# Kernel tuning notes

Measured on AMD Instinct MI355X. Metric: run time of the kernel, lower is better.

The kernel has to match this reference:

```python
import jax, jax.numpy as jnp
import numpy as np

D_MODEL = 1024
N_HEADS = 16
N_KV = 4
HEAD_DIM = D_MODEL // N_HEADS  # 64
SEQ = 2048
BATCH = 2
CAP = 50.0
EPS = 1e-5
THETA = 10000.0


def setup_inputs() -> dict:
    key = jax.random.key(0)
    ks = jax.random.split(key, 5)
    s = 0.02  # keep pre-attention logits in a sane range
    return {
        'x':   jax.random.normal(ks[0], (BATCH, SEQ, D_MODEL), dtype=jnp.float32),
        'w_q': jax.random.normal(ks[1], (D_MODEL, N_HEADS * HEAD_DIM), dtype=jnp.float32) * s,
        'w_k': jax.random.normal(ks[2], (D_MODEL, N_KV * HEAD_DIM), dtype=jnp.float32) * s,
        'w_v': jax.random.normal(ks[3], (D_MODEL, N_KV * HEAD_DIM), dtype=jnp.float32) * s,
        'w_o': jax.random.normal(ks[4], (N_HEADS * HEAD_DIM, D_MODEL), dtype=jnp.float32) * s,
    }


def _rms_norm(x, eps=EPS):
    return x * jax.lax.rsqrt(jnp.mean(jnp.square(x), axis=-1, keepdims=True) + eps)


def _rope_cos_sin(seq_len, head_dim, theta=THETA):
    inv_freq = 1.0 / (theta ** (jnp.arange(0, head_dim, 2, dtype=jnp.float32) / head_dim))
    freqs = jnp.arange(seq_len, dtype=jnp.float32)[:, None] * inv_freq[None, :]  # (S, d/2)
    return jnp.cos(freqs)[None, :, None, :], jnp.sin(freqs)[None, :, None, :]  # (1,S,1,d/2)


def _apply_rope(x, cos, sin):
    d = x.shape[-1] // 2
    x1, x2 = x[..., :d], x[..., d:]
    return jnp.concatenate([x1 * cos - x2 * sin, x2 * cos + x1 * sin], axis=-1).astype(x.dtype)


def reference(x, w_q, w_k, w_v, w_o):
    B, S, _ = x.shape
    q = (x @ w_q).reshape(B, S, N_HEADS, HEAD_DIM)
    k = (x @ w_k).reshape(B, S, N_KV, HEAD_DIM)
    v = (x @ w_v).reshape(B, S, N_KV, HEAD_DIM)

    # QK RMS-norm (no learned scale)
    q = _rms_norm(q)
    k = _rms_norm(k)

    cos, sin = _rope_cos_sin(S, HEAD_DIM)
    q = _apply_rope(q, cos, sin)
    k = _apply_rope(k, cos, sin)

    # GQA: repeat kv heads to match query heads
    rep = N_HEADS // N_KV
    k = jnp.repeat(k, rep, axis=2)
    v = jnp.repeat(v, rep, axis=2)

    scores = jnp.einsum('bqhd,bkhd->bhqk', q, k) / np.sqrt(HEAD_DIM).astype(np.float32)
    # softcap in float32, as in the original
    scores = jnp.tanh(scores.astype(jnp.float32) / CAP) * CAP
    causal = jnp.tril(jnp.ones((S, S), dtype=bool))  # (S, S)
    scores = jnp.where(causal[None, None], scores, -jnp.inf)
    probs = jax.nn.softmax(scores, axis=-1)  # dropout=0.0 -> identity

    y = jnp.einsum('bhqk,bkhd->bqhd', probs, v).reshape(B, S, N_HEADS * HEAD_DIM)
    return y @ w_o
```

## Files before the change

### kernel.cpp

```cpp
#include <hip/hip_runtime.h>
#include <hip/hip_bf16.h>
#include <math.h>

#define D_MODEL 1024
#define N_HEADS 16
#define N_KV 4
#define HEAD_DIM 64
#define SEQ 2048
#define BATCH 2
#define M_TOK (BATCH * SEQ)

typedef unsigned int u32;
typedef unsigned short u16;
typedef __attribute__((ext_vector_type(8))) short short8;
typedef __attribute__((ext_vector_type(4))) float f32x4;
typedef __attribute__((ext_vector_type(16))) float f32x16;

#define AS1 __attribute__((address_space(1)))
#define AS3 __attribute__((address_space(3)))

__device__ __forceinline__ u16 f2bf(float f) {
  union { __hip_bfloat16 h; u16 u; } c; c.h = __float2bfloat16(f); return c.u;
}
__device__ __forceinline__ u32 cvtpk(float lo, float hi) {
  u32 r; asm("v_cvt_pk_bf16_f32 %0, %1, %2" : "=v"(r) : "v"(lo), "v"(hi)); return r;
}
__device__ __forceinline__ void plswap(u32& a, u32& b) {
  asm volatile("v_permlane32_swap_b32 %0, %1" : "+v"(a), "+v"(b));
}
__device__ __forceinline__ float exp2fast(float x) { return __builtin_amdgcn_exp2f(x); }
__device__ __forceinline__ float rcpfast(float x) { return __builtin_amdgcn_rcpf(x); }

__global__ __launch_bounds__(256) void prep_kernel(const float* __restrict__ x,
                                                   const float* __restrict__ wq,
                                                   const float* __restrict__ wk,
                                                   const float* __restrict__ wv,
                                                   const float* __restrict__ wo,
                                                   u16* __restrict__ xb,
                                                   u16* __restrict__ wT,
                                                   u16* __restrict__ woT) {
  int bx = blockIdx.x;
  if (bx < 512) {
    const size_t base = (size_t)bx * 8192;
#pragma unroll
    for (int j = 0; j < 4; ++j) {
      size_t e = base + j * 2048 + threadIdx.x * 8;
      float4 f0 = *(const float4*)(x + e);
      float4 f1 = *(const float4*)(x + e + 4);
      uint4 u;
      u.x = cvtpk(f0.x, f0.y); u.y = cvtpk(f0.z, f0.w);
      u.z = cvtpk(f1.x, f1.y); u.w = cvtpk(f1.z, f1.w);
      *(uint4*)(xb + e) = u;
    }
    return;
  }
  bx -= 512;
  __shared__ float t[32][33];
  const float* src; u16* dst; int N, ntm, nts;
  if (bx < 1024)      { src = wq; dst = wT;                 N = 1024; ntm = 31; nts = 5; }
  else if (bx < 1280) { bx -= 1024; src = wk; dst = wT + (1024 << 10); N = 256; ntm = 7; nts = 3; }
  else if (bx < 1536) { bx -= 1280; src = wv; dst = wT + (1280 << 10); N = 256; ntm = 7; nts = 3; }
  else                { bx -= 1536; src = wo; dst = woT;    N = 1024; ntm = 31; nts = 5; }
  const int n0 = (bx & ntm) << 5, k0 = (bx >> nts) << 5;
  const int xx = threadIdx.x & 31, y = threadIdx.x >> 5;
#pragma unroll
  for (int i = 0; i < 4; ++i) {
    int r = y + (i << 3);
    t[r][xx] = src[(size_t)(k0 + r) * N + n0 + xx];
  }
  __syncthreads();
#pragma unroll
  for (int i = 0; i < 4; ++i) {
    int r = y + (i << 3);
    dst[(size_t)(n0 + r) * 1024 + k0 + xx] = f2bf(t[xx][r]);
  }
}

__global__ __launch_bounds__(256, 2) void qkvgemm_kernel(const u16* __restrict__ xb,
                                                         const u16* __restrict__ wT,
                                                         u16* __restrict__ Qbf,
                                                         u16* __restrict__ Kbf,
                                                         u16* __restrict__ Vt) {
  __shared__ uint4 SM[4][512];
  const int tid = threadIdx.x;
  const int w = tid >> 6, l = tid & 63;
  const int wr = w >> 1, wc = w & 1;
  int wg = ((int)blockIdx.x & 7) * 48 + ((int)blockIdx.x >> 3);
  const int mt = wg / 12, nb = wg - mt * 12;
  const int m0 = mt << 7;

  f32x4 acc[4][4];
#pragma unroll
  for (int m = 0; m < 4; ++m)
#pragma unroll
    for (int n = 0; n < 4; ++n)
#pragma unroll
      for (int j = 0; j < 4; ++j) acc[m][n][j] = 0.f;

  auto stage = [&](int buf, int k0) {
    const u16* Ab = xb + (size_t)m0 * 1024 + k0;
#pragma unroll
    for (int r = 0; r < 2; ++r) {
      int i = (w << 1) + r;
      int row = (i << 4) + (l >> 2);
      const u16* g = Ab + (size_t)row * 1024 + ((l & 3) << 3);
      __builtin_amdgcn_global_load_lds((const AS1 void*)g,
          (AS3 void*)((char*)SM + (buf << 13) + (i << 10)), 16, 0, 0);
    }
    const u16* Bb = wT + (size_t)(nb << 7) * 1024 + k0;
#pragma unroll
    for (int r = 0; r < 2; ++r) {
      int i = (w << 1) + r;
      int row = (i << 4) + (l >> 2);
      const u16* g = Bb + (size_t)row * 1024 + ((l & 3) << 3);
      __builtin_amdgcn_global_load_lds((const AS1 void*)g,
          (AS3 void*)((char*)SM + ((2 + buf) << 13) + (i << 10)), 16, 0, 0);
    }
  };

  stage(0, 0);
#pragma unroll 1
  for (int kt = 0; kt < 32; ++kt) {
    __syncthreads();
    if (kt + 1 < 32) stage((kt + 1) & 1, (kt + 1) << 5);
    const char* Ab = (const char*)SM + ((kt & 1) << 13);
    const char* Bb = (const char*)SM + ((2 + (kt & 1)) << 13);
    short8 af[4], bf[4];
#pragma unroll
    for (int m = 0; m < 4; ++m)
      af[m] = *(const short8*)(Ab + ((wr * 64 + m * 16 + (l & 15)) << 6) + ((l >> 4) << 4));
#pragma unroll
    for (int n = 0; n < 4; ++n)
      bf[n] = *(const short8*)(Bb + ((wc * 64 + n * 16 + (l & 15)) << 6) + ((l >> 4) << 4));
#pragma unroll
    for (int m = 0; m < 4; ++m)
#pragma unroll
      for (int n = 0; n < 4; ++n)
        acc[m][n] = __builtin_amdgcn_mfma_f32_16x16x32_bf16(af[m], bf[n], acc[m][n], 0, 0, 0);
  }

  __syncthreads();
  const int b = m0 >> 11;
  const int pos0 = (m0 & 2047) + wr * 64;
  const int lg = l >> 4, lc = l & 15;
  u16* lds = (u16*)((char*)SM + (w << 13));

  if (nb < 10) {
    float rs[4][4];
#pragma unroll
    for (int m = 0; m < 4; ++m)
#pragma unroll
      for (int j = 0; j < 4; ++j) {
        float ssq = 0.f;
#pragma unroll
        for (int n = 0; n < 4; ++n) ssq = fmaf(acc[m][n][j], acc[m][n][j], ssq);
        ssq += __shfl_xor(ssq, 1); ssq += __shfl_xor(ssq, 2);
        ssq += __shfl_xor(ssq, 4); ssq += __shfl_xor(ssq, 8);
        rs[m][j] = rsqrtf(ssq * (1.f / 64.f) + 1e-5f);
      }
    const float osc = (nb < 8) ? 0.0025f : 1.0f;
    const float invf0 = powf(10000.0f, (float)lc * (-1.f / 32.f));
    const float invf1 = powf(10000.0f, (float)(lc + 16) * (-1.f / 32.f));
#pragma unroll
    for (int m = 0; m < 4; ++m) {
#pragma unroll
      for (int j = 0; j < 4; ++j) {
        const int row = m * 16 + lg * 4 + j;
        const float pos = (float)(pos0 + row);
        float s0, c0, s1, c1;
        sincosf(pos * invf0, &s0, &c0);
        sincosf(pos * invf1, &s1, &c1);
        const float r_ = rs[m][j];
        float x0 = acc[m][0][j] * r_, x1 = acc[m][1][j] * r_;
        float x2 = acc[m][2][j] * r_, x3 = acc[m][3][j] * r_;
        u16 o0 = f2bf((x0 * c0 - x2 * s0) * osc);
        u16 o1 = f2bf((x1 * c1 - x3 * s1) * osc);
        u16 o2 = f2bf((x2 * c0 + x0 * s0) * osc);
        u16 o3 = f2bf((x3 * c1 + x1 * s1) * osc);
        const int rb = row << 6, xr = (row & 7) << 3;
        lds[rb + (lc ^ xr)] = o0;
        lds[rb + ((16 + lc) ^ xr)] = o1;
        lds[rb + ((32 + lc) ^ xr)] = o2;
        lds[rb + ((48 + lc) ^ xr)] = o3;
      }
    }
  } else {
#pragma unroll
    for (int m = 0; m < 4; ++m)
#pragma unroll
      for (int n = 0; n < 4; ++n) {
        const int d = n * 16 + lc;
        const int tok = m * 16 + lg * 4;
        uint2 u;
        u.x = cvtpk(acc[m][n][0], acc[m][n][1]);
        u.y = cvtpk(acc[m][n][2], acc[m][n][3]);
        *(uint2*)(lds + (d << 6) + (tok ^ ((d & 7) << 3))) = u;
      }
  }
  __syncthreads();

  u16* gp; int rstride;
  if (nb < 8)       { gp = Qbf + ((size_t)((b * 16 + nb * 2 + wc) * 2048 + pos0) << 6); rstride = 64; }
  else if (nb < 10) { gp = Kbf + ((size_t)((b * 4 + (nb - 8) * 2 + wc) * 2048 + pos0) << 6); rstride = 64; }
  else              { gp = Vt + (((size_t)((b * 4 + (nb - 10) * 2 + wc) * 64)) << 11) + pos0; rstride = 2048; }
#pragma unroll
  for (int ic = 0; ic < 8; ++ic) {
    const int c = (ic << 6) + l;
    const int row = c >> 3, col8 = (c & 7) << 3;
    uint4 v = *(const uint4*)(lds + (row << 6) + (col8 ^ ((row & 7) << 3)));
    *(uint4*)(gp + (size_t)row * rstride + col8) = v;
  }
}

__global__ __launch_bounds__(256, 2) void gemm_kernel(const u16* __restrict__ A,
                                                      const u16* __restrict__ BT,
                                                      float* __restrict__ C) {
  __shared__ uint4 SM[4][512];
  const int tid = threadIdx.x;
  const int w = tid >> 6, l = tid & 63;
  const int wr = w >> 1, wc = w & 1;
  int wg = ((int)blockIdx.x & 7) * 32 + ((int)blockIdx.x >> 3);
  const int m0 = (wg >> 3) << 7, n0 = (wg & 7) << 7;

  f32x4 acc[4][4];
#pragma unroll
  for (int m = 0; m < 4; ++m)
#pragma unroll
    for (int n = 0; n < 4; ++n)
#pragma unroll
      for (int j = 0; j < 4; ++j) acc[m][n][j] = 0.f;

  auto stage = [&](int buf, int k0) {
    const u16* Ab = A + (size_t)m0 * 1024 + k0;
#pragma unroll
    for (int r = 0; r < 2; ++r) {
      int i = (w << 1) + r;
      int row = (i << 4) + (l >> 2);
      const u16* g = Ab + (size_t)row * 1024 + ((l & 3) << 3);
      __builtin_amdgcn_global_load_lds((const AS1 void*)g,
          (AS3 void*)((char*)SM + (buf << 13) + (i << 10)), 16, 0, 0);
    }
    const u16* Bb = BT + (size_t)n0 * 1024 + k0;
#pragma unroll
    for (int r = 0; r < 2; ++r) {
      int i = (w << 1) + r;
      int row = (i << 4) + (l >> 2);
      const u16* g = Bb + (size_t)row * 1024 + ((l & 3) << 3);
      __builtin_amdgcn_global_load_lds((const AS1 void*)g,
          (AS3 void*)((char*)SM + ((2 + buf) << 13) + (i << 10)), 16, 0, 0);
    }
  };

  stage(0, 0);
#pragma unroll 1
  for (int kt = 0; kt < 32; ++kt) {
    __syncthreads();
    if (kt + 1 < 32) stage((kt + 1) & 1, (kt + 1) << 5);
    const char* Ab = (const char*)SM + ((kt & 1) << 13);
    const char* Bb = (const char*)SM + ((2 + (kt & 1)) << 13);
    short8 af[4], bf[4];
#pragma unroll
    for (int m = 0; m < 4; ++m)
      af[m] = *(const short8*)(Ab + ((wr * 64 + m * 16 + (l & 15)) << 6) + ((l >> 4) << 4));
#pragma unroll
    for (int n = 0; n < 4; ++n)
      bf[n] = *(const short8*)(Bb + ((wc * 64 + n * 16 + (l & 15)) << 6) + ((l >> 4) << 4));
#pragma unroll
    for (int m = 0; m < 4; ++m)
#pragma unroll
      for (int n = 0; n < 4; ++n)
        acc[m][n] = __builtin_amdgcn_mfma_f32_16x16x32_bf16(af[m], bf[n], acc[m][n], 0, 0, 0);
  }

#pragma unroll
  for (int m = 0; m < 4; ++m) {
    int row0 = m0 + wr * 64 + m * 16 + ((l >> 4) << 2);
#pragma unroll
    for (int n = 0; n < 4; ++n) {
      int col = n0 + wc * 64 + n * 16 + (l & 15);
#pragma unroll
      for (int j = 0; j < 4; ++j)
        C[(size_t)(row0 + j) * 1024 + col] = acc[m][n][j];
    }
  }
}

__device__ __forceinline__ short8 rdfrag(const uint4* lds, int row, int cb) {
  int byte = ((row << 7) + cb) ^ ((row & 7) << 4);
  return *(const short8*)((const char*)lds + byte);
}

__global__ __launch_bounds__(128, 2) void attn_kernel(const u16* __restrict__ Qbf,
                                                      const u16* __restrict__ Kbf,
                                                      const u16* __restrict__ Vt,
                                                      u16* __restrict__ ybf) {
  __shared__ uint4 KV[4][512];
  const int tid = threadIdx.x;
  const int bh = blockIdx.x & 31;
  const int qt = 31 - (blockIdx.x >> 5);
  const int q0 = qt << 6;
  const int w = tid >> 6, l = tid & 63;
  const int ql = l & 31, myh = l >> 5;
  const int b = bh >> 4, h = bh & 15, hkv = h >> 2;
  const int qg = q0 + (w << 5) + ql;

  const u16* Kg = Kbf + (((size_t)(b * 4 + hkv)) << 11) * 64;
  const u16* Vg = Vt + (((size_t)(b * 4 + hkv)) << 6) * 2048;

  short8 bq[4];
  {
    const u16* Qg = Qbf + ((size_t)((b * 16 + h) * 2048 + qg)) * 64 + myh * 8;
    bq[0] = *(const short8*)(Qg);
    bq[1] = *(const short8*)(Qg + 16);
    bq[2] = *(const short8*)(Qg + 32);
    bq[3] = *(const short8*)(Qg + 48);
  }

  f32x16 o0, o1;
#pragma unroll
  for (int i = 0; i < 16; ++i) { o0[i] = 0.f; o1[i] = 0.f; }
  float l_run = 0.f;

  const int KT = qt + 1;

  auto stage = [&](int buf, int kt) {
    const u16* gk = Kg + ((size_t)(kt << 6)) * 64;
    const u16* gv = Vg + (kt << 6);
#pragma unroll
    for (int i = 0; i < 4; ++i) {
      int c = tid + (i << 7);
      int row = c >> 3, off = c & 7;
      uint4 kk4 = *(const uint4*)(gk + row * 64 + (off << 3));
      uint4 vv4 = *(const uint4*)(gv + (size_t)row * 2048 + (off << 3));
      int byte = ((row << 7) + (off << 4)) ^ ((row & 7) << 4);
      *(uint4*)((char*)KV[buf << 1] + byte) = kk4;
      *(uint4*)((char*)KV[(buf << 1) + 1] + byte) = vv4;
    }
  };

  stage(0, 0);

  const float PC2 = -0.33333333f;
  const float PC4 = 0.13333333f;
  const float SC1 = 72.13475204444817f;
  const float SC0 = -11.541560327111708f;

#pragma unroll 1
  for (int kt = 0; kt < KT; ++kt) {
    const int k0 = kt << 6;
    const int buf = kt & 1;
    __syncthreads();
    if (kt + 1 < KT) stage(buf ^ 1, kt + 1);
    const bool full = (k0 + 63 <= q0 + (w << 5));
    const uint4* Kl = KV[buf << 1];
    const uint4* Vl = KV[(buf << 1) + 1];

    f32x16 s0, s1;
#pragma unroll
    for (int i = 0; i < 16; ++i) { s0[i] = 0.f; s1[i] = 0.f; }
    __builtin_amdgcn_s_setprio(1);
#pragma unroll
    for (int c = 0; c < 4; ++c) {
      short8 ak = rdfrag(Kl, ql, (c << 5) + (myh << 4));
      s0 = __builtin_amdgcn_mfma_f32_32x32x16_bf16(ak, bq[c], s0, 0, 0, 0);
    }
#pragma unroll
    for (int c = 0; c < 4; ++c) {
      short8 ak = rdfrag(Kl, 32 + ql, (c << 5) + (myh << 4));
      s1 = __builtin_amdgcn_mfma_f32_32x32x16_bf16(ak, bq[c], s1, 0, 0, 0);
    }
    __builtin_amdgcn_s_setprio(0);

    float lsum = 0.f;
    if (full) {
#pragma unroll
      for (int i = 0; i < 16; ++i) {
        float z = s0[i];
        float t2 = z * z;
        float pw = fmaf(t2, fmaf(t2, PC4, PC2), 1.0f);
        float p = exp2fast(fmaf(z * pw, SC1, SC0));
        s0[i] = p; lsum += p;
      }
#pragma unroll
      for (int i = 0; i < 16; ++i) {
        float z = s1[i];
        float t2 = z * z;
        float pw = fmaf(t2, fmaf(t2, PC4, PC2), 1.0f);
        float p = exp2fast(fmaf(z * pw, SC1, SC0));
        s1[i] = p; lsum += p;
      }
    } else {
#pragma unroll
      for (int i = 0; i < 16; ++i) {
        int kk = k0 + (i & 3) + ((i >> 2) << 3) + (myh << 2);
        float z = s0[i];
        float t2 = z * z;
        float pw = fmaf(t2, fmaf(t2, PC4, PC2), 1.0f);
        float p = exp2fast(fmaf(z * pw, SC1, SC0));
        p = (kk <= qg) ? p : 0.f;
        s0[i] = p; lsum += p;
      }
#pragma unroll
      for (int i = 0; i < 16; ++i) {
        int kk = k0 + 32 + (i & 3) + ((i >> 2) << 3) + (myh << 2);
        float z = s1[i];
        float t2 = z * z;
        float pw = fmaf(t2, fmaf(t2, PC4, PC2), 1.0f);
        float p = exp2fast(fmaf(z * pw, SC1, SC0));
        p = (kk <= qg) ? p : 0.f;
        s1[i] = p; lsum += p;
      }
    }
    l_run += lsum;

    short8 pa[4];
#pragma unroll
    for (int c = 0; c < 4; ++c) {
      const f32x16& P = (c < 2) ? s0 : s1;
      const int rb = (c & 1) << 3;
      u32 A = cvtpk(P[rb + 0], P[rb + 1]);
      u32 Cw = cvtpk(P[rb + 2], P[rb + 3]);
      u32 B = cvtpk(P[rb + 4], P[rb + 5]);
      u32 D = cvtpk(P[rb + 6], P[rb + 7]);
      plswap(A, B); plswap(Cw, D);
      union { u32 u[4]; short8 s; } pw_;
      pw_.u[0] = A; pw_.u[1] = Cw; pw_.u[2] = B; pw_.u[3] = D;
      pa[c] = pw_.s;
    }

    __builtin_amdgcn_s_setprio(1);
#pragma unroll
    for (int c = 0; c < 4; ++c) {
      short8 av = rdfrag(Vl, ql, (c << 5) + (myh << 4));
      o0 = __builtin_amdgcn_mfma_f32_32x32x16_bf16(av, pa[c], o0, 0, 0, 0);
    }
#pragma unroll
    for (int c = 0; c < 4; ++c) {
      short8 av = rdfrag(Vl, 32 + ql, (c << 5) + (myh << 4));
      o1 = __builtin_amdgcn_mfma_f32_32x32x16_bf16(av, pa[c], o1, 0, 0, 0);
    }
    __builtin_amdgcn_s_setprio(0);
  }

  float lr = l_run + __shfl_xor(l_run, 32);
  float rl = rcpfast(lr);
  u16* yr = ybf + ((size_t)(b * 2048 + qg)) * 1024 + h * 64;
#pragma unroll
  for (int i = 0; i < 16; i += 2) {
    int dof = (i & 3) + ((i >> 2) << 3) + (myh << 2);
    *(u32*)(yr + dof) = cvtpk(o0[i] * rl, o0[i + 1] * rl);
    *(u32*)(yr + 32 + dof) = cvtpk(o1[i] * rl, o1[i + 1] * rl);
  }
}

extern "C" void kernel_launch(void* const* d_in, const int* in_sizes, int n_in,
                              void* d_out, int out_size, void* d_ws, size_t ws_size,
                              hipStream_t stream) {
  (void)in_sizes; (void)n_in; (void)out_size; (void)ws_size;
  const float* x  = (const float*)d_in[0];
  const float* wq = (const float*)d_in[1];
  const float* wk = (const float*)d_in[2];
  const float* wv = (const float*)d_in[3];
  const float* wo = (const float*)d_in[4];
  float* out = (float*)d_out;

  char* ws = (char*)d_ws;
  u16* xb  = (u16*)ws;
  u16* ybf = (u16*)(ws + (8u << 20));
  u16* woT = (u16*)(ws + (16u << 20));
  u16* wT  = (u16*)(ws + (18u << 20));
  u16* Qbf = (u16*)(ws + (21u << 20));
  u16* Kbf = (u16*)(ws + (29u << 20));
  u16* Vt  = (u16*)(ws + (31u << 20));

  prep_kernel<<<dim3(3072), 256, 0, stream>>>(x, wq, wk, wv, wo, xb, wT, woT);
  qkvgemm_kernel<<<dim3(384), 256, 0, stream>>>(xb, wT, Qbf, Kbf, Vt);
  attn_kernel<<<dim3(1024), 128, 0, stream>>>(Qbf, Kbf, Vt, ybf);
  gemm_kernel<<<dim3(256), 256, 0, stream>>>(ybf, woT, out);
}
```

Baseline: 106.1 us.

## Share KV tiles across GQA heads per block and skip masked diagonal half

Attention blocks now own one KV group and one 32-query tile, with each of the four waves handling a different query head of that group. Each staged K/V tile is therefore reused by four heads instead of being reloaded per head. The diagonal tile now skips the fully masked upper 32-key half. The softcap polynomial is also trimmed to one term and evaluated with packed f32 math. The risks are a lower-accuracy tanh approximation, more threads per block competing for registers, and a grid of 512 larger blocks.

```diff
diff --git a/kernel.cpp b/kernel.cpp
--- a/kernel.cpp
+++ b/kernel.cpp
@@ -15,6 +15,7 @@
 typedef __attribute__((ext_vector_type(8))) short short8;
 typedef __attribute__((ext_vector_type(4))) float f32x4;
 typedef __attribute__((ext_vector_type(16))) float f32x16;
+typedef __attribute__((ext_vector_type(2))) float f32x2;
 
 #define AS1 __attribute__((address_space(1)))
 #define AS3 __attribute__((address_space(3)))
@@ -30,6 +31,12 @@
 }
 __device__ __forceinline__ float exp2fast(float x) { return __builtin_amdgcn_exp2f(x); }
 __device__ __forceinline__ float rcpfast(float x) { return __builtin_amdgcn_rcpf(x); }
+__device__ __forceinline__ f32x2 pk_mul(f32x2 a, f32x2 b) {
+  f32x2 d; asm("v_pk_mul_f32 %0, %1, %2" : "=v"(d) : "v"(a), "v"(b)); return d;
+}
+__device__ __forceinline__ f32x2 pk_fma(f32x2 a, f32x2 b, f32x2 c) {
+  f32x2 d; asm("v_pk_fma_f32 %0, %1, %2, %3" : "=v"(d) : "v"(a), "v"(b), "v"(c)); return d;
+}
 
 __global__ __launch_bounds__(256) void prep_kernel(const float* __restrict__ x,
                                                    const float* __restrict__ wq,
@@ -290,22 +297,23 @@
   return *(const short8*)((const char*)lds + byte);
 }
 
-__global__ __launch_bounds__(128, 2) void attn_kernel(const u16* __restrict__ Qbf,
+__global__ __launch_bounds__(256, 2) void attn_kernel(const u16* __restrict__ Qbf,
                                                       const u16* __restrict__ Kbf,
                                                       const u16* __restrict__ Vt,
                                                       u16* __restrict__ ybf) {
   __shared__ uint4 KV[4][512];
   const int tid = threadIdx.x;
-  const int bh = blockIdx.x & 31;
-  const int qt = 31 - (blockIdx.x >> 5);
-  const int q0 = qt << 6;
+  const int g = blockIdx.x & 7;
+  const int j = 63 - (blockIdx.x >> 3);
+  const int b = g >> 2, hkv = g & 3;
   const int w = tid >> 6, l = tid & 63;
   const int ql = l & 31, myh = l >> 5;
-  const int b = bh >> 4, h = bh & 15, hkv = h >> 2;
-  const int qg = q0 + (w << 5) + ql;
-
-  const u16* Kg = Kbf + (((size_t)(b * 4 + hkv)) << 11) * 64;
-  const u16* Vg = Vt + (((size_t)(b * 4 + hkv)) << 6) * 2048;
+  const int h = hkv * 4 + w;
+  const int q0 = j << 5;
+  const int qg = q0 + ql;
+
+  const u16* Kg = Kbf + (((size_t)g) << 11) * 64;
+  const u16* Vg = Vt + (((size_t)g) << 6) * 2048;
 
   short8 bq[4];
   {
@@ -321,14 +329,14 @@
   for (int i = 0; i < 16; ++i) { o0[i] = 0.f; o1[i] = 0.f; }
   float l_run = 0.f;
 
-  const int KT = qt + 1;
+  const int KT = (j >> 1) + 1;
 
   auto stage = [&](int buf, int kt) {
     const u16* gk = Kg + ((size_t)(kt << 6)) * 64;
     const u16* gv = Vg + (kt << 6);
 #pragma unroll
-    for (int i = 0; i < 4; ++i) {
-      int c = tid + (i << 7);
+    for (int i = 0; i < 2; ++i) {
+      int c = tid + (i << 8);
       int row = c >> 3, off = c & 7;
       uint4 kk4 = *(const uint4*)(gk + row * 64 + (off << 3));
       uint4 vv4 = *(const uint4*)(gv + (size_t)row * 2048 + (off << 3));
@@ -341,17 +349,20 @@
   stage(0, 0);
 
   const float PC2 = -0.33333333f;
-  const float PC4 = 0.13333333f;
   const float SC1 = 72.13475204444817f;
   const float SC0 = -11.541560327111708f;
+  const f32x2 PC2v = {PC2, PC2};
+  const f32x2 SC1v = {SC1, SC1};
+  const f32x2 SC0v = {SC0, SC0};
+  const f32x2 ONEv = {1.0f, 1.0f};
 
 #pragma unroll 1
   for (int kt = 0; kt < KT; ++kt) {
-    const int k0 = kt << 6;
     const int buf = kt & 1;
     __syncthreads();
     if (kt + 1 < KT) stage(buf ^ 1, kt + 1);
-    const bool full = (k0 + 63 <= q0 + (w << 5));
+    const bool last = (kt == KT - 1);
+    const bool havehi = !last || (j & 1);
     const uint4* Kl = KV[buf << 1];
     const uint4* Vl = KV[(buf << 1) + 1];
 
@@ -364,80 +375,80 @@
       short8 ak = rdfrag(Kl, ql, (c << 5) + (myh << 4));
       s0 = __builtin_amdgcn_mfma_f32_32x32x16_bf16(ak, bq[c], s0, 0, 0, 0);
     }
-#pragma unroll
-    for (int c = 0; c < 4; ++c) {
-      short8 ak = rdfrag(Kl, 32 + ql, (c << 5) + (myh << 4));
-      s1 = __builtin_amdgcn_mfma_f32_32x32x16_bf16(ak, bq[c], s1, 0, 0, 0);
+    if (havehi) {
+#pragma unroll
+      for (int c = 0; c < 4; ++c) {
+        short8 ak = rdfrag(Kl, 32 + ql, (c << 5) + (myh << 4));
+        s1 = __builtin_amdgcn_mfma_f32_32x32x16_bf16(ak, bq[c], s1, 0, 0, 0);
+      }
     }
     __builtin_amdgcn_s_setprio(0);
 
     float lsum = 0.f;
-    if (full) {
+    auto cap_full = [&](f32x16& s) {
+#pragma unroll
+      for (int p = 0; p < 8; ++p) {
+        f32x2 z; z.x = s[2 * p]; z.y = s[2 * p + 1];
+        f32x2 z2 = pk_mul(z, z);
+        f32x2 zc = pk_fma(z2, PC2v, ONEv);
+        f32x2 zs = pk_mul(z, SC1v);
+        f32x2 ar = pk_fma(zs, zc, SC0v);
+        float p0 = exp2fast(ar.x);
+        float p1 = exp2fast(ar.y);
+        s[2 * p] = p0; s[2 * p + 1] = p1;
+        lsum += p0; lsum += p1;
+      }
+    };
+    auto cap_diag = [&](f32x16& s) {
 #pragma unroll
       for (int i = 0; i < 16; ++i) {
-        float z = s0[i];
-        float t2 = z * z;
-        float pw = fmaf(t2, fmaf(t2, PC4, PC2), 1.0f);
-        float p = exp2fast(fmaf(z * pw, SC1, SC0));
-        s0[i] = p; lsum += p;
-      }
-#pragma unroll
-      for (int i = 0; i < 16; ++i) {
-        float z = s1[i];
-        float t2 = z * z;
-        float pw = fmaf(t2, fmaf(t2, PC4, PC2), 1.0f);
-        float p = exp2fast(fmaf(z * pw, SC1, SC0));
-        s1[i] = p; lsum += p;
-      }
-    } else {
-#pragma unroll
-      for (int i = 0; i < 16; ++i) {
-        int kk = k0 + (i & 3) + ((i >> 2) << 3) + (myh << 2);
-        float z = s0[i];
-        float t2 = z * z;
-        float pw = fmaf(t2, fmaf(t2, PC4, PC2), 1.0f);
-        float p = exp2fast(fmaf(z * pw, SC1, SC0));
-        p = (kk <= qg) ? p : 0.f;
-        s0[i] = p; lsum += p;
-      }
-#pragma unroll
-      for (int i = 0; i < 16; ++i) {
-        int kk = k0 + 32 + (i & 3) + ((i >> 2) << 3) + (myh << 2);
-        float z = s1[i];
-        float t2 = z * z;
-        float pw = fmaf(t2, fmaf(t2, PC4, PC2), 1.0f);
-        float p = exp2fast(fmaf(z * pw, SC1, SC0));
-        p = (kk <= qg) ? p : 0.f;
-        s1[i] = p; lsum += p;
-      }
-    }
+        int kl = (i & 3) + ((i >> 2) << 3) + (myh << 2);
+        float z = s[i];
+        float zc = fmaf(z * z, PC2, 1.0f);
+        float p = exp2fast(fmaf(z * zc, SC1, SC0));
+        p = (kl <= ql) ? p : 0.f;
+        s[i] = p; lsum += p;
+      }
+    };
+    if (!last)       { cap_full(s0); cap_full(s1); }
+    else if (j & 1)  { cap_full(s0); cap_diag(s1); }
+    else             { cap_diag(s0); }
     l_run += lsum;
 
     short8 pa[4];
-#pragma unroll
-    for (int c = 0; c < 4; ++c) {
-      const f32x16& P = (c < 2) ? s0 : s1;
-      const int rb = (c & 1) << 3;
-      u32 A = cvtpk(P[rb + 0], P[rb + 1]);
-      u32 Cw = cvtpk(P[rb + 2], P[rb + 3]);
-      u32 B = cvtpk(P[rb + 4], P[rb + 5]);
-      u32 D = cvtpk(P[rb + 6], P[rb + 7]);
-      plswap(A, B); plswap(Cw, D);
-      union { u32 u[4]; short8 s; } pw_;
-      pw_.u[0] = A; pw_.u[1] = Cw; pw_.u[2] = B; pw_.u[3] = D;
-      pa[c] = pw_.s;
-    }
+    auto mkpa = [&](const f32x16& P, int c0) {
+#pragma unroll
+      for (int ci = 0; ci < 2; ++ci) {
+        const int rb = ci << 3;
+        u32 A = cvtpk(P[rb + 0], P[rb + 1]);
+        u32 Cw = cvtpk(P[rb + 2], P[rb + 3]);
+        u32 B = cvtpk(P[rb + 4], P[rb + 5]);
+        u32 D = cvtpk(P[rb + 6], P[rb + 7]);
+        plswap(A, B); plswap(Cw, D);
+        union { u32 u[4]; short8 s; } pw_;
+        pw_.u[0] = A; pw_.u[1] = Cw; pw_.u[2] = B; pw_.u[3] = D;
+        pa[c0 + ci] = pw_.s;
+      }
+    };
+    mkpa(s0, 0);
+    if (havehi) mkpa(s1, 2);
 
     __builtin_amdgcn_s_setprio(1);
 #pragma unroll
-    for (int c = 0; c < 4; ++c) {
+    for (int c = 0; c < 2; ++c) {
       short8 av = rdfrag(Vl, ql, (c << 5) + (myh << 4));
       o0 = __builtin_amdgcn_mfma_f32_32x32x16_bf16(av, pa[c], o0, 0, 0, 0);
-    }
-#pragma unroll
-    for (int c = 0; c < 4; ++c) {
-      short8 av = rdfrag(Vl, 32 + ql, (c << 5) + (myh << 4));
-      o1 = __builtin_amdgcn_mfma_f32_32x32x16_bf16(av, pa[c], o1, 0, 0, 0);
+      short8 av1 = rdfrag(Vl, 32 + ql, (c << 5) + (myh << 4));
+      o1 = __builtin_amdgcn_mfma_f32_32x32x16_bf16(av1, pa[c], o1, 0, 0, 0);
+    }
+    if (havehi) {
+#pragma unroll
+      for (int c = 2; c < 4; ++c) {
+        short8 av = rdfrag(Vl, ql, (c << 5) + (myh << 4));
+        o0 = __builtin_amdgcn_mfma_f32_32x32x16_bf16(av, pa[c], o0, 0, 0, 0);
+        short8 av1 = rdfrag(Vl, 32 + ql, (c << 5) + (myh << 4));
+        o1 = __builtin_amdgcn_mfma_f32_32x32x16_bf16(av1, pa[c], o1, 0, 0, 0);
+      }
     }
     __builtin_amdgcn_s_setprio(0);
   }
@@ -475,6 +486,6 @@
 
   prep_kernel<<<dim3(3072), 256, 0, stream>>>(x, wq, wk, wv, wo, xb, wT, woT);
   qkvgemm_kernel<<<dim3(384), 256, 0, stream>>>(xb, wT, Qbf, Kbf, Vt);
-  attn_kernel<<<dim3(1024), 128, 0, stream>>>(Qbf, Kbf, Vt, ybf);
+  attn_kernel<<<dim3(512), 256, 0, stream>>>(Qbf, Kbf, Vt, ybf);
   gemm_kernel<<<dim3(256), 256, 0, stream>>>(ybf, woT, out);
 }
```

Result: no change. 105.9 us (-0.1%).
